# Kernel tuning notes

Hardware: AMD Instinct MI355X
Metric: run time of the kernel (lower is better)

## Reference

```python
import jax, jax.numpy as jnp
import numpy as np

EPS_RMS = 1e-6
EPS_NORM = 1e-9


def rmsnorm(x):
    return x * jax.lax.rsqrt(jnp.mean(x * x, axis=-1, keepdims=True) + EPS_RMS)


def apply_rotary(x, cos, sin):
    # x: [b, h, s, d]; cos/sin: [1, 1, s, d//2]
    d2 = x.shape[-1] // 2
    x1, x2 = x[..., :d2], x[..., d2:]
    return jnp.concatenate([x1 * cos - x2 * sin, x1 * sin + x2 * cos], axis=-1)


def setup_inputs() -> dict:
    key = jax.random.key(0)
    ks = jax.random.split(key, 16)
    b, l, e, h = 4, 1024, 2048, 16
    d = e // h
    query = jax.random.normal(ks[0], (b, l, e), jnp.float32)
    keyt = jax.random.normal(ks[1], (b, l, e), jnp.float32)
    value = jax.random.normal(ks[2], (b, l, e), jnp.float32)
    attn_mask = jnp.tril(jnp.ones((l, l), bool))[None, None]  # causal bool mask
    cos = jax.random.normal(ks[3], (1, 1, l, d // 2), jnp.float32)
    sin = jax.random.normal(ks[4], (1, 1, l, d // 2), jnp.float32)
    sc = 0.02
    Wq = jax.random.normal(ks[5], (e, e), jnp.float32) * sc
    bq = jnp.zeros((e,), jnp.float32)
    Wk = jax.random.normal(ks[6], (e, e), jnp.float32) * sc
    bk = jnp.zeros((e,), jnp.float32)
    Wv = jax.random.normal(ks[7], (e, e), jnp.float32) * sc
    bv = jnp.zeros((e,), jnp.float32)
    Wo = jax.random.normal(ks[8], (e, e), jnp.float32) * sc
    bo = jnp.zeros((e,), jnp.float32)
    return dict(query=query, key=keyt, value=value, attn_mask=attn_mask,
                cos=cos, sin=sin, Wq=Wq, bq=bq, Wk=Wk, bk=bk,
                Wv=Wv, bv=bv, Wo=Wo, bo=bo)


def reference(query, key, value, attn_mask, cos, sin, Wq, bq, Wk, bk, Wv, bv, Wo, bo):
    b, l, e = query.shape
    s = key.shape[1]
    h = 16
    d = e // h
    q = (query @ Wq.T + bq).reshape(b, l, h, d).transpose(0, 2, 1, 3)
    k = (key @ Wk.T + bk).reshape(b, s, h, d).transpose(0, 2, 1, 3)
    v = (value @ Wv.T + bv).reshape(b, s, h, d).transpose(0, 2, 1, 3)
    q, k = rmsnorm(q), rmsnorm(k)
    # rotary (self-attention, s == l)
    q = apply_rotary(q, cos[:, :, :s], sin[:, :, :s])
    k = apply_rotary(k, cos[:, :, :s], sin[:, :, :s])
    # SDPA with boolean mask
    scores = jnp.einsum('bhld,bhsd->bhls', q, k) / jnp.sqrt(jnp.float32(d))
    scores = jnp.where(attn_mask, scores, jnp.finfo(scores.dtype).min)
    p = jax.nn.softmax(scores, axis=-1)
    o = jnp.einsum('bhls,bhsd->bhld', p, v)  # [b,h,l,d]
    # post-attention v-orthogonalization (o.shape == v.shape here)
    vnorm = jnp.sqrt(jnp.sum(v * v, axis=-1, keepdims=True))
    vn = v / jnp.maximum(vnorm, EPS_NORM)
    o = o - jnp.sum(o * vn, axis=-1, keepdims=True) * vn
    o = o.transpose(0, 2, 1, 3).reshape(b, l, e)
    return o @ Wo.T + bo
```

## Files before the change

### kernel.cpp

```cpp
#include <hip/hip_runtime.h>

typedef short short8 __attribute__((ext_vector_type(8)));
typedef float f32x4 __attribute__((ext_vector_type(4)));

#define MFMA_BF16 __builtin_amdgcn_mfma_f32_16x16x32_bf16

__device__ __forceinline__ unsigned short f2bf(float f) {
  unsigned int u = __float_as_uint(f);
  u += 0x7fffu + ((u >> 16) & 1u);
  return (unsigned short)(u >> 16);
}
__device__ __forceinline__ float bf2f(unsigned short u) {
  return __uint_as_float(((unsigned int)u) << 16);
}

typedef __attribute__((address_space(1))) const unsigned int as1_u32;
typedef __attribute__((address_space(3))) unsigned int as3_u32;
__device__ __forceinline__ void gld16(const void* g, void* l) {
  __builtin_amdgcn_global_load_lds((as1_u32*)(unsigned long long)g,
                                   (as3_u32*)(unsigned int)(unsigned long long)l,
                                   16, 0, 0);
}

struct CvtArgs {
  const float* s[7];
  unsigned short* d[7];
  int n8[7];
};

__global__ __launch_bounds__(256) void cvtall(CvtArgs a) {
  const int seg = blockIdx.y;
  int i = blockIdx.x * 256 + threadIdx.x;
  if (i >= a.n8[seg]) return;
  const float4* s4 = (const float4*)a.s[seg];
  float4 x = s4[2 * i], y = s4[2 * i + 1];
  short8 o = {(short)f2bf(x.x), (short)f2bf(x.y), (short)f2bf(x.z), (short)f2bf(x.w),
              (short)f2bf(y.x), (short)f2bf(y.y), (short)f2bf(y.z), (short)f2bf(y.w)};
  *(short8*)&a.d[seg][(size_t)i * 8] = o;
}

struct GemmArgs {
  const unsigned short* A[3];
  const unsigned short* W[3];
  const float* bias[3];
  unsigned short* Cb[3];
  float* Cf;
};

template <bool OUTBF, int NZ>
__global__ __launch_bounds__(256) void gemm_bf16(GemmArgs g) {
  const int B = blockIdx.x;
  const int xcd = B & 7;
  const int i = B >> 3;
  const int z = i >> 6;
  const int r = i & 63;
  const int xb = r >> 4, inner = r & 15;
  const int bn = (xb * 4 + (inner & 3)) * 128;
  const int bm = (xcd * 4 + (inner >> 2)) * 128;
  const int K = 2048, N = 2048;

  const unsigned short* A = g.A[z];
  const unsigned short* W = g.W[z];
  const float* bias = g.bias[z];
  unsigned short* Cb = g.Cb[z];

  __shared__ unsigned short As[128 * 64];
  __shared__ unsigned short Bs[128 * 64];
  const int t = threadIdx.x, lane = t & 63, w = t >> 6;
  const int wr = w >> 1, wc = w & 1;
  const int quad = lane >> 4, l16 = lane & 15;

  const int srow = lane >> 3;
  const int sk = (lane & 7) * 8;
  size_t ga[4], gb[4];
  unsigned short *la[4], *lb[4];
  for (int j = 0; j < 4; ++j) {
    int rr = (w * 4 + j) * 8 + srow;
    ga[j] = (size_t)(bm + rr) * K + sk;
    gb[j] = (size_t)(bn + rr) * K + sk;
    la[j] = &As[(w * 4 + j) * 512];
    lb[j] = &Bs[(w * 4 + j) * 512];
  }

  const f32x4 fz = {0.f, 0.f, 0.f, 0.f};
  f32x4 acc[4][4];
  for (int a = 0; a < 4; ++a)
    for (int b = 0; b < 4; ++b) acc[a][b] = fz;

  for (int k0 = 0; k0 < K; k0 += 64) {
    __syncthreads();
    for (int j = 0; j < 4; ++j) {
      gld16(A + ga[j] + k0, la[j]);
      gld16(W + gb[j] + k0, lb[j]);
    }
    __syncthreads();
    for (int kk = 0; kk < 2; ++kk) {
      short8 af[4], bfv[4];
      for (int mt = 0; mt < 4; ++mt)
        af[mt] = *(const short8*)&As[(wr * 64 + mt * 16 + l16) * 64 + kk * 32 + quad * 8];
      for (int nt = 0; nt < 4; ++nt)
        bfv[nt] = *(const short8*)&Bs[(wc * 64 + nt * 16 + l16) * 64 + kk * 32 + quad * 8];
      for (int mt = 0; mt < 4; ++mt)
        for (int nt = 0; nt < 4; ++nt)
          acc[mt][nt] = MFMA_BF16(af[mt], bfv[nt], acc[mt][nt], 0, 0, 0);
    }
  }

  for (int mt = 0; mt < 4; ++mt)
    for (int nt = 0; nt < 4; ++nt) {
      int row = bm + wr * 64 + mt * 16 + quad * 4;
      int col = bn + wc * 64 + nt * 16 + l16;
      float bc = bias[col];
      for (int r2 = 0; r2 < 4; ++r2) {
        float v = acc[mt][nt][r2] + bc;
        if (OUTBF) Cb[(size_t)(row + r2) * N + col] = f2bf(v);
        else       g.Cf[(size_t)(row + r2) * N + col] = v;
      }
    }
}

__global__ __launch_bounds__(256) void rmsvt(
    const unsigned short* __restrict__ Qf, const unsigned short* __restrict__ Kf,
    const unsigned short* __restrict__ Vf,
    const float* __restrict__ cosT, const float* __restrict__ sinT,
    unsigned short* __restrict__ Qb, unsigned short* __restrict__ Kb,
    unsigned short* __restrict__ Vt) {
  __shared__ unsigned short Vsh[64 * 136];
  if (blockIdx.x < 16384) {
    const int rid = blockIdx.x * 4 + (threadIdx.x >> 6);
    const int lane = threadIdx.x & 63;
    const int li = rid & 1023;
    const int bh = rid >> 10;
    const int hi = bh & 15, bi = bh >> 4;
    const int src = (bi * 1024 + li) * 2048 + hi * 128;
    const int dst = rid * 128;
    const float c = cosT[li * 64 + lane];
    const float s = sinT[li * 64 + lane];

    float q1 = bf2f(Qf[src + lane]), q2 = bf2f(Qf[src + 64 + lane]);
    float ss = q1 * q1 + q2 * q2;
    for (int off = 32; off; off >>= 1) ss += __shfl_xor(ss, off, 64);
    float r = rsqrtf(ss * (1.f / 128.f) + 1e-6f);
    float qa = q1 * r, qb2 = q2 * r;
    const float qsc = 0.08838834764831845f * 1.4426950408889634f;
    Qb[dst + lane]      = f2bf((qa * c - qb2 * s) * qsc);
    Qb[dst + 64 + lane] = f2bf((qa * s + qb2 * c) * qsc);

    float k1 = bf2f(Kf[src + lane]), k2 = bf2f(Kf[src + 64 + lane]);
    float ks = k1 * k1 + k2 * k2;
    for (int off = 32; off; off >>= 1) ks += __shfl_xor(ks, off, 64);
    float rk = rsqrtf(ks * (1.f / 128.f) + 1e-6f);
    float ka = k1 * rk, kb2 = k2 * rk;
    Kb[dst + lane]      = f2bf(ka * c - kb2 * s);
    Kb[dst + 64 + lane] = f2bf(ka * s + kb2 * c);
  } else {
    const int bid = blockIdx.x - 16384;
    const int t = threadIdx.x;
    const int bh = bid >> 4, l0 = (bid & 15) * 64;
    const int hi = bh & 15, bi = bh >> 4;
    {
      int row = t >> 2, c4 = t & 3;
      const unsigned short* src = &Vf[(size_t)(bi * 1024 + l0 + row) * 2048 + hi * 128];
      for (int i = 0; i < 4; ++i) {
        int chunk = c4 * 4 + i;
        *(int4*)&Vsh[row * 136 + chunk * 8] = *(const int4*)&src[chunk * 8];
      }
    }
    __syncthreads();
    {
      int d = t >> 1, half = t & 1;
      unsigned short* dst = &Vt[(size_t)bh * 131072 + (size_t)d * 1024 + l0 + half * 32];
      for (int g = 0; g < 4; ++g) {
        short8 o;
        for (int j = 0; j < 8; ++j)
          o[j] = (short)Vsh[(half * 32 + g * 8 + j) * 136 + d];
        *(short8*)&dst[g * 8] = o;
      }
    }
  }
}

__global__ __launch_bounds__(512, 4) void attn(
    const unsigned short* __restrict__ Qb, const unsigned short* __restrict__ Kb,
    const unsigned short* __restrict__ Vt, unsigned short* __restrict__ Of0,
    unsigned short* __restrict__ Of1, float* __restrict__ Lb) {
  __shared__ unsigned short Kl[64 * 136];
  __shared__ unsigned short Vl[128 * 72];
  __shared__ unsigned short Pl[8][16 * 72];
  const int t = threadIdx.x, lane = t & 63, w = t >> 6;
  const int quad = lane >> 4, l16 = lane & 15;
  const int B = blockIdx.x;
  const int bh = (B & 7) + 8 * ((B >> 3) & 7);
  const int jj = B >> 6;
  const int pair = jj >> 1, split = jj & 1;
  const unsigned short* Qh = Qb + (size_t)bh * 131072;
  const unsigned short* Kh = Kb + (size_t)bh * 131072;
  const unsigned short* Vh = Vt + (size_t)bh * 131072;
  unsigned short* Oh = (split ? Of1 : Of0) + (size_t)bh * 131072;
  float* Lh = Lb + split * 65536 + bh * 1024;

  const int krow = t >> 4, kcol = (t & 15) * 8;
  const int vdr = t >> 3, vc = (t & 7) * 8;
  const f32x4 fz = {0.f, 0.f, 0.f, 0.f};

  for (int ti = 0; ti < 2; ++ti) {
    const int qt = ti == 0 ? 7 - pair : pair;
    const int q0 = qt * 128;

    short8 aQ[4];
    {
      int qr = q0 + w * 16 + l16;
      for (int kk = 0; kk < 4; ++kk)
        aQ[kk] = *(const short8*)&Qh[(size_t)qr * 128 + kk * 32 + quad * 8];
    }
    f32x4 oacc[8];
    for (int i = 0; i < 8; ++i) oacc[i] = fz;
    float Lr[4] = {0.f, 0.f, 0.f, 0.f};
    const int nST = 2 * qt + 2;

    for (int st = split; st < nST; st += 2) {
      const int s0 = st * 64;
      __syncthreads();
      {
        *(int4*)&Kl[krow * 136 + kcol] =
            *(const int4*)&Kh[(size_t)(s0 + krow) * 128 + kcol];
        *(int4*)&Kl[(krow + 32) * 136 + kcol] =
            *(const int4*)&Kh[(size_t)(s0 + krow + 32) * 128 + kcol];
        *(int4*)&Vl[vdr * 72 + vc] =
            *(const int4*)&Vh[(size_t)vdr * 1024 + s0 + vc];
        *(int4*)&Vl[(vdr + 64) * 72 + vc] =
            *(const int4*)&Vh[(size_t)(vdr + 64) * 1024 + s0 + vc];
      }
      __syncthreads();

      f32x4 sfr[4];
      for (int j = 0; j < 4; ++j) sfr[j] = fz;
      for (int kk = 0; kk < 4; ++kk)
        for (int ni = 0; ni < 4; ++ni) {
          short8 bK = *(const short8*)&Kl[(ni * 16 + l16) * 136 + kk * 32 + quad * 8];
          sfr[ni] = MFMA_BF16(aQ[kk], bK, sfr[ni], 0, 0, 0);
        }

      const bool diag = (s0 + 63 > q0);
      for (int r = 0; r < 4; ++r) {
        int q = q0 + w * 16 + quad * 4 + r;
        float ps = 0.f;
        for (int ni = 0; ni < 4; ++ni) {
          float sv = sfr[ni][r];
          if (diag && (s0 + ni * 16 + l16 > q)) sv = -30000.f;
          float pp = exp2f(sv - 16.5f);
          ps += pp;
          Pl[w][(quad * 4 + r) * 72 + ni * 16 + l16] = f2bf(pp);
        }
        ps += __shfl_xor(ps, 1, 64);
        ps += __shfl_xor(ps, 2, 64);
        ps += __shfl_xor(ps, 4, 64);
        ps += __shfl_xor(ps, 8, 64);
        Lr[r] += ps;
      }

      for (int kk = 0; kk < 2; ++kk) {
        short8 aP = *(const short8*)&Pl[w][l16 * 72 + kk * 32 + quad * 8];
        for (int nt = 0; nt < 8; ++nt) {
          short8 bV = *(const short8*)&Vl[(nt * 16 + l16) * 72 + kk * 32 + quad * 8];
          oacc[nt] = MFMA_BF16(aP, bV, oacc[nt], 0, 0, 0);
        }
      }
    }

    for (int r = 0; r < 4; ++r) {
      int q = q0 + w * 16 + quad * 4 + r;
      size_t base = (size_t)q * 128;
      for (int nt = 0; nt < 8; ++nt)
        Oh[base + nt * 16 + l16] = f2bf(oacc[nt][r]);
      if (l16 == 0) Lh[q] = Lr[r];
    }
  }
}

__global__ __launch_bounds__(256) void vnfix(
    const unsigned short* __restrict__ Of0, const unsigned short* __restrict__ Of1,
    const float* __restrict__ Lb, const unsigned short* __restrict__ Vf,
    unsigned short* __restrict__ Op) {
  const int rid = blockIdx.x * 4 + (threadIdx.x >> 6);
  const int lane = threadIdx.x & 63;
  const int li = rid & 1023;
  const int bh = rid >> 10;
  const int hi = bh & 15, bi = bh >> 4;
  const int src = (bi * 1024 + li) * 2048 + hi * 128;
  float inv = 1.f / (Lb[rid] + Lb[65536 + rid]);
  float o1 = (bf2f(Of0[(size_t)rid * 128 + lane]) + bf2f(Of1[(size_t)rid * 128 + lane])) * inv;
  float o2 = (bf2f(Of0[(size_t)rid * 128 + 64 + lane]) + bf2f(Of1[(size_t)rid * 128 + 64 + lane])) * inv;
  float v1 = bf2f(Vf[src + lane]), v2 = bf2f(Vf[src + 64 + lane]);
  float vv = v1 * v1 + v2 * v2;
  float dd = o1 * v1 + o2 * v2;
  for (int off = 32; off; off >>= 1) {
    vv += __shfl_xor(vv, off, 64);
    dd += __shfl_xor(dd, off, 64);
  }
  float vn = fmaxf(sqrtf(vv), 1e-9f);
  float tc = dd / (vn * vn);
  Op[src + lane]      = f2bf(o1 - tc * v1);
  Op[src + 64 + lane] = f2bf(o2 - tc * v2);
}

extern "C" void kernel_launch(void* const* d_in, const int* in_sizes, int n_in,
                              void* d_out, int out_size, void* d_ws, size_t ws_size,
                              hipStream_t stream) {
  const float* query = (const float*)d_in[0];
  const float* key   = (const float*)d_in[1];
  const float* value = (const float*)d_in[2];
  const float* cosT  = (const float*)d_in[4];
  const float* sinT  = (const float*)d_in[5];
  const float* Wq = (const float*)d_in[6];
  const float* bq = (const float*)d_in[7];
  const float* Wk = (const float*)d_in[8];
  const float* bk = (const float*)d_in[9];
  const float* Wv = (const float*)d_in[10];
  const float* bv = (const float*)d_in[11];
  const float* Wo = (const float*)d_in[12];
  const float* bo = (const float*)d_in[13];
  float* out = (float*)d_out;

  char* ws = (char*)d_ws;
  const size_t MB = 1048576;
  unsigned short* Xq  = (unsigned short*)(ws);
  unsigned short* Xk  = (unsigned short*)(ws + 16 * MB);
  unsigned short* Xv  = (unsigned short*)(ws + 32 * MB);
  unsigned short* Wqb = (unsigned short*)(ws + 48 * MB);
  unsigned short* Wkb = (unsigned short*)(ws + 56 * MB);
  unsigned short* Wvb = (unsigned short*)(ws + 64 * MB);
  unsigned short* Wob = (unsigned short*)(ws + 72 * MB);
  unsigned short* Qf  = (unsigned short*)(ws + 80 * MB);
  unsigned short* Kf  = (unsigned short*)(ws + 96 * MB);
  unsigned short* Vf  = (unsigned short*)(ws + 112 * MB);
  unsigned short* Qbb = Xq;
  unsigned short* Kbb = Xk;
  unsigned short* Vtb = Xv;
  unsigned short* Of0 = Qf;
  unsigned short* Of1 = Kf;
  float*          Lbp = (float*)(ws + 64 * MB);
  unsigned short* Opb = (unsigned short*)(ws + 48 * MB);

  CvtArgs ca;
  ca.s[0] = query; ca.d[0] = Xq;  ca.n8[0] = 1048576;
  ca.s[1] = key;   ca.d[1] = Xk;  ca.n8[1] = 1048576;
  ca.s[2] = value; ca.d[2] = Xv;  ca.n8[2] = 1048576;
  ca.s[3] = Wq;    ca.d[3] = Wqb; ca.n8[3] = 524288;
  ca.s[4] = Wk;    ca.d[4] = Wkb; ca.n8[4] = 524288;
  ca.s[5] = Wv;    ca.d[5] = Wvb; ca.n8[5] = 524288;
  ca.s[6] = Wo;    ca.d[6] = Wob; ca.n8[6] = 524288;
  cvtall<<<dim3(4096, 7), 256, 0, stream>>>(ca);

  GemmArgs gp;
  gp.A[0] = Xq;  gp.A[1] = Xk;  gp.A[2] = Xv;
  gp.W[0] = Wqb; gp.W[1] = Wkb; gp.W[2] = Wvb;
  gp.bias[0] = bq; gp.bias[1] = bk; gp.bias[2] = bv;
  gp.Cb[0] = Qf; gp.Cb[1] = Kf; gp.Cb[2] = Vf;
  gp.Cf = nullptr;
  gemm_bf16<true, 3><<<1536, 256, 0, stream>>>(gp);

  rmsvt<<<17408, 256, 0, stream>>>(Qf, Kf, Vf, cosT, sinT, Qbb, Kbb, Vtb);

  attn<<<512, 512, 0, stream>>>(Qbb, Kbb, Vtb, Of0, Of1, Lbp);

  vnfix<<<16384, 256, 0, stream>>>(Of0, Of1, Lbp, Vf, Opb);

  GemmArgs go;
  go.A[0] = Opb; go.A[1] = nullptr; go.A[2] = nullptr;
  go.W[0] = Wob; go.W[1] = nullptr; go.W[2] = nullptr;
  go.bias[0] = bo; go.bias[1] = nullptr; go.bias[2] = nullptr;
  go.Cb[0] = nullptr; go.Cb[1] = nullptr; go.Cb[2] = nullptr;
  go.Cf = out;
  gemm_bf16<false, 1><<<512, 256, 0, stream>>>(go);
}
```

Baseline: 474.4 us.

## Rework projection GEMM into 256x128 tiles with 4-stage async LDS ring

The bf16 GEMM used for the QKV and output projections changes from 128x128 tiles with 256 threads to 256x128 tiles with 512 threads. It now uses a 4-deep ring of K=32 slices in dynamic shared memory, filled by direct global-to-LDS loads issued three stages ahead. Raw s_waitcnt/s_barrier calls replace the two __syncthreads per step, an XOR swizzle reduces LDS bank conflicts, and MFMA sections are raised with s_setprio. The aim is to hide global load latency and halve synchronisation per K step. The cost is 96KB of LDS per block, which limits occupancy to one block per CU, and fewer blocks in the grid.

Result: faster. 430.1 us (-9.3%).

```diff
diff --git a/kernel.cpp b/kernel.cpp
--- a/kernel.cpp
+++ b/kernel.cpp
@@ -20,6 +20,13 @@
   __builtin_amdgcn_global_load_lds((as1_u32*)(unsigned long long)g,
                                    (as3_u32*)(unsigned int)(unsigned long long)l,
                                    16, 0, 0);
+}
+
+#define VMCNT(n) asm volatile("s_waitcnt vmcnt(" #n ")" ::: "memory")
+__device__ __forceinline__ void barrier_raw() {
+  asm volatile("" ::: "memory");
+  __builtin_amdgcn_s_barrier();
+  asm volatile("" ::: "memory");
 }
 
 struct CvtArgs {
@@ -48,63 +55,81 @@
 };
 
 template <bool OUTBF, int NZ>
-__global__ __launch_bounds__(256) void gemm_bf16(GemmArgs g) {
+__global__ __launch_bounds__(512, 2) void gemm_bf16(GemmArgs g) {
+  extern __shared__ unsigned short Sh[];
   const int B = blockIdx.x;
-  const int xcd = B & 7;
-  const int i = B >> 3;
-  const int z = i >> 6;
-  const int r = i & 63;
-  const int xb = r >> 4, inner = r & 15;
-  const int bn = (xb * 4 + (inner & 3)) * 128;
-  const int bm = (xcd * 4 + (inner >> 2)) * 128;
-  const int K = 2048, N = 2048;
-
-  const unsigned short* A = g.A[z];
-  const unsigned short* W = g.W[z];
-  const float* bias = g.bias[z];
-  unsigned short* Cb = g.Cb[z];
-
-  __shared__ unsigned short As[128 * 64];
-  __shared__ unsigned short Bs[128 * 64];
+  const int z = B >> 8;
+  const int i = B & 255;
+  const int xcd = i & 7;
+  const int q = i >> 3;
+  const int bn = (q >> 1) * 128;
+  const int bm = (xcd * 2 + (q & 1)) * 256;
+  const int K = 2048, N = 2048, NT = 64;
+  const int RS = 12288;
+
+  const unsigned short* __restrict__ A = g.A[z];
+  const unsigned short* __restrict__ W = g.W[z];
+  const float* __restrict__ bias = g.bias[z];
+  unsigned short* __restrict__ Cb = g.Cb[z];
+
   const int t = threadIdx.x, lane = t & 63, w = t >> 6;
   const int wr = w >> 1, wc = w & 1;
   const int quad = lane >> 4, l16 = lane & 15;
 
-  const int srow = lane >> 3;
-  const int sk = (lane & 7) * 8;
-  size_t ga[4], gb[4];
-  unsigned short *la[4], *lb[4];
-  for (int j = 0; j < 4; ++j) {
-    int rr = (w * 4 + j) * 8 + srow;
-    ga[j] = (size_t)(bm + rr) * K + sk;
-    gb[j] = (size_t)(bn + rr) * K + sk;
-    la[j] = &As[(w * 4 + j) * 512];
-    lb[j] = &Bs[(w * 4 + j) * 512];
-  }
+  const int sk = ((lane & 3) * 8) ^ (((lane >> 3) & 3) << 3);
+  const int srow = lane >> 2;
+  const size_t gA0 = (size_t)(bm + w * 32 + srow) * K + sk;
+  const size_t gA1 = (size_t)(bm + w * 32 + 16 + srow) * K + sk;
+  const size_t gB  = (size_t)(bn + w * 16 + srow) * K + sk;
+  const int lA0 = (w * 32) * 32;
+  const int lA1 = (w * 32 + 16) * 32;
+  const int lB  = 8192 + (w * 16) * 32;
+
+#define STAGE(tt, ring)                                   \
+  do {                                                    \
+    const int kq = (tt) * 32;                             \
+    unsigned short* Ld = &Sh[(ring) * RS];                \
+    gld16(A + gA0 + kq, Ld + lA0);                        \
+    gld16(A + gA1 + kq, Ld + lA1);                        \
+    gld16(W + gB + kq, Ld + lB);                          \
+  } while (0)
+
+  const int ka = (quad * 8) ^ (((l16 >> 1) & 3) << 3);
+  const int raA = (wr * 64 + l16) * 32 + ka;
+  const int raB = 8192 + (wc * 64 + l16) * 32 + ka;
 
   const f32x4 fz = {0.f, 0.f, 0.f, 0.f};
   f32x4 acc[4][4];
   for (int a = 0; a < 4; ++a)
     for (int b = 0; b < 4; ++b) acc[a][b] = fz;
 
-  for (int k0 = 0; k0 < K; k0 += 64) {
-    __syncthreads();
-    for (int j = 0; j < 4; ++j) {
-      gld16(A + ga[j] + k0, la[j]);
-      gld16(W + gb[j] + k0, lb[j]);
-    }
-    __syncthreads();
-    for (int kk = 0; kk < 2; ++kk) {
-      short8 af[4], bfv[4];
-      for (int mt = 0; mt < 4; ++mt)
-        af[mt] = *(const short8*)&As[(wr * 64 + mt * 16 + l16) * 64 + kk * 32 + quad * 8];
+  STAGE(0, 0);
+  STAGE(1, 1);
+  STAGE(2, 2);
+  VMCNT(6);
+  barrier_raw();
+
+#pragma unroll 4
+  for (int tt = 0; tt < NT; ++tt) {
+    const unsigned short* Sr = &Sh[(tt & 3) * RS];
+    short8 af[4], bv[4];
+    for (int mt = 0; mt < 4; ++mt)
+      af[mt] = *(const short8*)&Sr[raA + mt * 512];
+    for (int nt = 0; nt < 4; ++nt)
+      bv[nt] = *(const short8*)&Sr[raB + nt * 512];
+    if (tt + 3 < NT) STAGE(tt + 3, (tt + 3) & 3);
+    barrier_raw();
+    __builtin_amdgcn_s_setprio(1);
+    for (int mt = 0; mt < 4; ++mt)
       for (int nt = 0; nt < 4; ++nt)
-        bfv[nt] = *(const short8*)&Bs[(wc * 64 + nt * 16 + l16) * 64 + kk * 32 + quad * 8];
-      for (int mt = 0; mt < 4; ++mt)
-        for (int nt = 0; nt < 4; ++nt)
-          acc[mt][nt] = MFMA_BF16(af[mt], bfv[nt], acc[mt][nt], 0, 0, 0);
-    }
+        acc[mt][nt] = MFMA_BF16(af[mt], bv[nt], acc[mt][nt], 0, 0, 0);
+    __builtin_amdgcn_s_setprio(0);
+    if (tt < NT - 3) VMCNT(6);
+    else if (tt == NT - 3) VMCNT(3);
+    else if (tt == NT - 2) VMCNT(0);
+    barrier_raw();
   }
+#undef STAGE
 
   for (int mt = 0; mt < 4; ++mt)
     for (int nt = 0; nt < 4; ++nt) {
@@ -358,7 +383,7 @@
   gp.bias[0] = bq; gp.bias[1] = bk; gp.bias[2] = bv;
   gp.Cb[0] = Qf; gp.Cb[1] = Kf; gp.Cb[2] = Vf;
   gp.Cf = nullptr;
-  gemm_bf16<true, 3><<<1536, 256, 0, stream>>>(gp);
+  gemm_bf16<true, 3><<<768, 512, 98304, stream>>>(gp);
 
   rmsvt<<<17408, 256, 0, stream>>>(Qf, Kf, Vf, cosT, sinT, Qbb, Kbb, Vtb);
 
@@ -372,5 +397,5 @@
   go.bias[0] = bo; go.bias[1] = nullptr; go.bias[2] = nullptr;
   go.Cb[0] = nullptr; go.Cb[1] = nullptr; go.Cb[2] = nullptr;
   go.Cf = out;
-  gemm_bf16<false, 1><<<512, 256, 0, stream>>>(go);
-}
+  gemm_bf16<false, 1><<<256, 512, 98304, stream>>>(go);
+}
```
